# Kernel tuning notes

Measured on AMD Instinct MI355X. Metric: run time of the kernel, lower is better.

The kernel has to match this reference:

```python
import jax, jax.numpy as jnp
import numpy as np

N, E, C, A, R, HID = 10000, 160000, 128, 10, 8, 32
D_NODE = C * 4           # 128x0e + 128x1o -> 128 + 128*3
D_MID = 2 * C + 2 * C * 3  # irreps_mid = 2x128x0e + 2x128x1o -> 1024
AVG_NEIGH = 16.0
SQRT3 = 1.7320508075688772


def _linear_irreps(s, v, W0, W1):
    # e3nn-style per-irrep Linear: scalars [n,u]->[n,v], vectors [n,u,3]->[n,v,3]
    f = 1.0 / np.sqrt(W0.shape[0]).astype(np.float32)
    return s @ W0 * f, jnp.einsum('num,uv->nvm', v, W1) * f


def setup_inputs() -> dict:
    key = jax.random.key(0)
    ks = jax.random.split(key, 18)
    g = lambda i, sh: jax.random.normal(ks[i], sh, jnp.float32)
    return dict(
        node_attrs=g(0, (N, A)),
        node_feats=g(1, (N, D_NODE)),
        edge_attrs=g(2, (E, 4)),  # SH lmax=1: [Y00, Y1(-1..1)] (e3nn y,z,x order)
        edge_feats=jax.random.uniform(ks[3], (E, R), jnp.float32),
        edge_index=jax.random.randint(ks[4], (2, E), 0, N),
        W_up0=g(5, (C, C)), W_up1=g(6, (C, C)),
        Wr1=g(7, (R, 64)), Wr2=g(8, (64, 64)), Wr3=g(9, (64, 64)), Wr4=g(10, (64, 4 * C)),
        W_se1=g(11, (D_MID, HID)), W_se2=g(12, (HID, D_MID)),
        W_lin0=g(13, (2 * C, C)), W_lin1=g(14, (2 * C, C)),
        W_sk0=g(15, (C, A, C)), W_sk1=g(16, (C, A, C)),
    )


def reference(node_attrs, node_feats, edge_attrs, edge_feats, edge_index,
              W_up0, W_up1, Wr1, Wr2, Wr3, Wr4, W_se1, W_se2,
              W_lin0, W_lin1, W_sk0, W_sk1):
    n = node_feats.shape[0]
    e = edge_attrs.shape[0]
    s_in = node_feats[:, :C]
    v_in = node_feats[:, C:].reshape(n, C, 3)
    # linear_up (node_feats_irreps -> edge_irreps)
    s, v = _linear_irreps(s_in, v_in, W_up0, W_up1)
    # radial MLP (FullyConnectedNet, silu) -> per-edge TP weights [E, 4, C]
    h = edge_feats
    for W in (Wr1, Wr2, Wr3):
        h = jax.nn.silu(h @ W / np.sqrt(W.shape[0]).astype(np.float32))
    tpw = (h @ Wr4 / np.sqrt(Wr4.shape[0]).astype(np.float32)).reshape(e, 4, C)
    src, dst = edge_index[0], edge_index[1]
    ss, vv = s[src], v[src]          # gather source-node features per edge
    y0 = edge_attrs[:, 0]
    y1 = edge_attrs[:, 1:4]
    # equivariant TensorProduct (uvu, per-edge learned weights), 4 instructions
    m1 = tpw[:, 0] * ss * y0[:, None]                          # 0e x 0e -> 0e
    m2 = (tpw[:, 1] * ss)[:, :, None] * y1[:, None, :]         # 0e x 1o -> 1o
    m3 = tpw[:, 2][:, :, None] * vv * y0[:, None, None]        # 1o x 0e -> 1o
    m4 = tpw[:, 3] * jnp.einsum('eum,em->eu', vv, y1) / SQRT3  # 1o x 1o -> 0e
    S_m = jnp.concatenate([m1, m4], 1)       # [E, 2C] scalar part of irreps_mid
    V_m = jnp.concatenate([m2, m3], 1)       # [E, 2C, 3] vector part
    # SE attention gate on flattened edge messages (squeeze-excitation)
    mji = jnp.concatenate([S_m, V_m.reshape(e, -1)], 1)  # [E, 1024]
    gate = jax.nn.sigmoid(jax.nn.silu(mji @ W_se1) @ W_se2)
    mji = mji * gate
    S_m = mji[:, :2 * C]
    V_m = mji[:, 2 * C:].reshape(e, 2 * C, 3)
    # scatter-sum messages to destination nodes
    S_n = jax.ops.segment_sum(S_m, dst, num_segments=n)
    V_n = jax.ops.segment_sum(V_m, dst, num_segments=n)
    # linear (irreps_mid -> target), divided by avg_num_neighbors
    S_n, V_n = _linear_irreps(S_n, V_n, W_lin0, W_lin1)
    S_n = S_n / AVG_NEIGH
    V_n = V_n / AVG_NEIGH
    # skip_tp: FullyConnectedTensorProduct(target x 10x0e -> target)
    f = 1.0 / np.sqrt(C * A).astype(np.float32)
    S_o = jnp.einsum('nu,nw,uwv->nv', S_n, node_attrs, W_sk0) * f
    V_o = jnp.einsum('num,nw,uwv->nvm', V_n, node_attrs, W_sk1) * f
    # reshape_irreps -> [n, channels=C, 1+3]
    return jnp.concatenate([S_o[:, :, None], V_o], axis=2)
```

## Files before the change

### kernel.cpp

```cpp
#include <hip/hip_runtime.h>
#include <hip/hip_bf16.h>

#define N_NODES 10000
#define N_EDGES 160000

typedef __bf16 bf16x8 __attribute__((ext_vector_type(8)));
typedef float  f32x4  __attribute__((ext_vector_type(4)));
typedef unsigned short u16x8 __attribute__((ext_vector_type(8)));
union U16x8 { u16x8 u; bf16x8 b; };

__device__ __forceinline__ float sigf(float x){ return 1.0f/(1.0f+__expf(-x)); }
__device__ __forceinline__ float siluf(float x){ return x*sigf(x); }

__device__ __forceinline__ unsigned int f2bfbits(float f){
  unsigned int u = __float_as_uint(f);
  return (u + 0x7fffu + ((u>>16)&1u)) >> 16;
}
__device__ __forceinline__ void split3(float v, unsigned short* h, unsigned short* m, unsigned short* lo){
  unsigned int hb = f2bfbits(v); float hf = __uint_as_float(hb<<16);
  float r1 = v - hf;
  unsigned int mb = f2bfbits(r1); float mf = __uint_as_float(mb<<16);
  unsigned int lb = f2bfbits(r1 - mf);
  *h=(unsigned short)hb; *m=(unsigned short)mb; *lo=(unsigned short)lb;
}

__device__ __forceinline__ int dmap(int dp){
  int c = dp>>3, slot = dp&7;
  if (slot==0) return c;
  if (slot==1) return 128+c;
  if (slot<5)  return 256+3*c+(slot-2);
  return 640+3*c+(slot-5);
}

__global__ void pack_weights(const float* __restrict__ Wr4,
                             const float* __restrict__ Wse1,
                             const float* __restrict__ Wse2,
                             unsigned short* __restrict__ wr4pk,
                             unsigned short* __restrict__ wse1pk,
                             unsigned short* __restrict__ wse2pk)
{
  int t = blockIdx.x*256 + threadIdx.x;
  int j = t&7, l = (t>>3)&63;
  int lg = l>>4, lm = l&15;
  {
    int ks = (t>>9)&1; int nt = t>>10;
    int k = ks*32 + lg*8 + j;
    int col = nt*16 + lm;
    split3(Wr4[k*512+col]*0.125f, wr4pk+t, wr4pk+t+32768, wr4pk+t+65536);
  }
  {
    int kb = (t>>9)&31; int nt = t>>14;
    int d = dmap(kb*32 + lg*8 + j);
    int col = nt*16 + lm;
    split3(Wse1[d*32+col], wse1pk+t, wse1pk+t+32768, wse1pk+t+65536);
  }
  {
    int nt = t>>9;
    int krow = lg*8 + j;
    int d = dmap(nt*16 + lm);
    split3(Wse2[krow*1024+d], wse2pk+t, wse2pk+t+32768, wse2pk+t+65536);
  }
}

__global__ __launch_bounds__(128) void node_up_kernel(
    const float* __restrict__ nf, const float* __restrict__ W0, const float* __restrict__ W1,
    float* __restrict__ s_up, float* __restrict__ v_up)
{
  int n = blockIdx.x; int c = threadIdx.x;
  __shared__ float row[512];
  #pragma unroll
  for (int i=0;i<4;i++) row[c + 128*i] = nf[n*512 + c + 128*i];
  __syncthreads();
  float as=0.f, a0=0.f, a1=0.f, a2=0.f;
  for (int u=0;u<128;u++){
    float w0 = W0[u*128+c], w1 = W1[u*128+c];
    as += row[u]*w0;
    a0 += row[128+u*3+0]*w1;
    a1 += row[128+u*3+1]*w1;
    a2 += row[128+u*3+2]*w1;
  }
  const float f = 0.08838834764831845f;
  s_up[n*128+c] = as*f;
  v_up[n*384 + c*3+0] = a0*f;
  v_up[n*384 + c*3+1] = a1*f;
  v_up[n*384 + c*3+2] = a2*f;
}

#define OFF_MJI  16384
#define OFF_H3H  81920
#define OFF_H3L  83968
#define OFF_SG1H 86016
#define OFF_SG1L 87040
#define OFF_SRC  88064
#define OFF_DST  88128
#define OFF_Y    88192

__global__ __launch_bounds__(1024, 1) void edge_kernel(
    const float* __restrict__ ef, const float* __restrict__ ea, const int* __restrict__ ei,
    const float* __restrict__ Wr1, const float* __restrict__ Wr2, const float* __restrict__ Wr3,
    const unsigned short* __restrict__ wr4pk, const unsigned short* __restrict__ wse1pk,
    const unsigned short* __restrict__ wse2pk,
    const float* __restrict__ s_up, const float* __restrict__ v_up, float* __restrict__ accg)
{
  __shared__ __align__(16) char smem[88448];
  float* hA = (float*)smem;
  float* hB = (float*)(smem + 4096);
  float* partial = (float*)smem;
  int*   s_src = (int*)(smem + OFF_SRC);
  int*   s_dst = (int*)(smem + OFF_DST);
  float* s_y   = (float*)(smem + OFF_Y);

  const int t = threadIdx.x;
  const int e0 = blockIdx.x * 16;
  const int l = t & 63, w = t >> 6;
  const int lg = l >> 4, lm = l & 15;

  auto mjivec = [&](int v) -> float* {
    int p = v ^ ((v>>3)&7) ^ ((v>>8)&7);
    return (float*)(smem + OFF_MJI + p*16);
  };

  if (t < 16){ s_src[t] = ei[e0+t]; s_dst[t] = ei[N_EDGES + e0 + t]; }
  else if (t >= 64 && t < 128){ int q=t-64; s_y[(q>>2)*4 + (q&3)] = ea[(e0+(q>>2))*4 + (q&3)]; }

  {
    const int i = t & 63, eh = t >> 6;
    float r;
    { float a0=0.f;
      #pragma unroll
      for (int k=0;k<8;k++) a0 += ef[(e0+eh)*8+k]*Wr1[k*64+i];
      r = siluf(a0*0.35355339059327373f);
    }
    hA[eh*64+i]=r;
    __syncthreads();
    { float a0=0.f;
      for (int k=0;k<64;k++) a0 += hA[eh*64+k]*Wr2[k*64+i];
      r = siluf(a0*0.125f);
    }
    hB[eh*64+i]=r;
    __syncthreads();
    { float a0=0.f;
      for (int k=0;k<64;k++) a0 += hB[eh*64+k]*Wr3[k*64+i];
      r = siluf(a0*0.125f);
    }
    unsigned int hb = f2bfbits(r);
    unsigned int lb = f2bfbits(r - __uint_as_float(hb<<16));
    int o = (eh*128 + i*2) ^ ((eh&7)<<4);
    *(unsigned short*)(smem + OFF_H3H + o) = (unsigned short)hb;
    *(unsigned short*)(smem + OFF_H3L + o) = (unsigned short)lb;
  }
  __syncthreads();

  if (w < 8) {
    int oa0 = (lm*128 +  0 + lg*16) ^ ((lm&7)<<4);
    int oa1 = (lm*128 + 64 + lg*16) ^ ((lm&7)<<4);
    bf16x8 a0h = *(const bf16x8*)(smem + OFF_H3H + oa0);
    bf16x8 a1h = *(const bf16x8*)(smem + OFF_H3H + oa1);
    bf16x8 a0l = *(const bf16x8*)(smem + OFF_H3L + oa0);
    bf16x8 a1l = *(const bf16x8*)(smem + OFF_H3L + oa1);
    f32x4 tq[4];
    #pragma unroll
    for (int q=0;q<4;q++){
      int nt = q*8 + w;
      const unsigned short* bp0 = wr4pk + (nt*2+0)*512 + l*8;
      const unsigned short* bp1 = wr4pk + (nt*2+1)*512 + l*8;
      bf16x8 b0h = *(const bf16x8*)(bp0);
      bf16x8 b0m = *(const bf16x8*)(bp0+32768);
      bf16x8 b0l = *(const bf16x8*)(bp0+65536);
      bf16x8 b1h = *(const bf16x8*)(bp1);
      bf16x8 b1m = *(const bf16x8*)(bp1+32768);
      bf16x8 b1l = *(const bf16x8*)(bp1+65536);
      f32x4 acc = {0.f,0.f,0.f,0.f};
      acc = __builtin_amdgcn_mfma_f32_16x16x32_bf16(a0h,b0h,acc,0,0,0);
      acc = __builtin_amdgcn_mfma_f32_16x16x32_bf16(a1h,b1h,acc,0,0,0);
      acc = __builtin_amdgcn_mfma_f32_16x16x32_bf16(a0h,b0m,acc,0,0,0);
      acc = __builtin_amdgcn_mfma_f32_16x16x32_bf16(a1h,b1m,acc,0,0,0);
      acc = __builtin_amdgcn_mfma_f32_16x16x32_bf16(a0h,b0l,acc,0,0,0);
      acc = __builtin_amdgcn_mfma_f32_16x16x32_bf16(a1h,b1l,acc,0,0,0);
      acc = __builtin_amdgcn_mfma_f32_16x16x32_bf16(a0l,b0h,acc,0,0,0);
      acc = __builtin_amdgcn_mfma_f32_16x16x32_bf16(a1l,b1h,acc,0,0,0);
      acc = __builtin_amdgcn_mfma_f32_16x16x32_bf16(a0l,b0m,acc,0,0,0);
      acc = __builtin_amdgcn_mfma_f32_16x16x32_bf16(a1l,b1m,acc,0,0,0);
      tq[q] = acc;
    }
    const int cc = w*16 + lm;
    #pragma unroll
    for (int r=0;r<4;r++){
      int e = lg*4 + r;
      int src = s_src[e];
      float y0=s_y[e*4+0], yx=s_y[e*4+1], yy=s_y[e*4+2], yz=s_y[e*4+3];
      float ss = s_up[src*128+cc];
      const float* vp = v_up + src*384 + cc*3;
      float vx=vp[0], vy=vp[1], vz=vp[2];
      float m1  = tq[0][r]*ss*y0;
      float t1s = tq[1][r]*ss;
      float t2y = tq[2][r]*y0;
      float m4  = tq[3][r]*(vx*yx+vy*yy+vz*yz)*0.5773502691896258f;
      int v0 = e*256 + cc*2;
      f32x4 o0; o0[0]=m1;     o0[1]=m4;     o0[2]=t1s*yx; o0[3]=t1s*yy;
      f32x4 o1; o1[0]=t1s*yz; o1[1]=t2y*vx; o1[2]=t2y*vy; o1[3]=t2y*vz;
      *(f32x4*)mjivec(v0)   = o0;
      *(f32x4*)mjivec(v0+1) = o1;
    }
  }
  __syncthreads();

  if (w < 8) {
    f32x4 acc0 = {0.f,0.f,0.f,0.f}, acc1 = {0.f,0.f,0.f,0.f};
    #pragma unroll
    for (int ik=0; ik<4; ik++){
      int kb = w*4 + ik;
      int v = lm*256 + kb*8 + lg*2;
      f32x4 fa = *(const f32x4*)mjivec(v);
      f32x4 fb = *(const f32x4*)mjivec(v+1);
      U16x8 ua;
      ua.u[0]=(unsigned short)f2bfbits(fa[0]); ua.u[1]=(unsigned short)f2bfbits(fa[1]);
      ua.u[2]=(unsigned short)f2bfbits(fa[2]); ua.u[3]=(unsigned short)f2bfbits(fa[3]);
      ua.u[4]=(unsigned short)f2bfbits(fb[0]); ua.u[5]=(unsigned short)f2bfbits(fb[1]);
      ua.u[6]=(unsigned short)f2bfbits(fb[2]); ua.u[7]=(unsigned short)f2bfbits(fb[3]);
      bf16x8 a = ua.b;
      #pragma unroll
      for (int p=0;p<3;p++){
        bf16x8 b0 = *(const bf16x8*)(wse1pk + p*32768 + (0*32+kb)*512 + l*8);
        bf16x8 b1 = *(const bf16x8*)(wse1pk + p*32768 + (1*32+kb)*512 + l*8);
        acc0 = __builtin_amdgcn_mfma_f32_16x16x32_bf16(a,b0,acc0,0,0,0);
        acc1 = __builtin_amdgcn_mfma_f32_16x16x32_bf16(a,b1,acc1,0,0,0);
      }
    }
    #pragma unroll
    for (int r=0;r<4;r++){
      int row = lg*4 + r;
      partial[(w*16+row)*32 + lm     ] = acc0[r];
      partial[(w*16+row)*32 + 16+lm  ] = acc1[r];
    }
  }
  __syncthreads();
  if (t < 512) {
    int e = t>>5, jj = t&31;
    float s = 0.f;
    #pragma unroll
    for (int w8=0; w8<8; w8++) s += partial[(w8*16+e)*32 + jj];
    float g1 = siluf(s);
    unsigned int hb = f2bfbits(g1);
    unsigned int lb = f2bfbits(g1 - __uint_as_float(hb<<16));
    *(unsigned short*)(smem + OFF_SG1H + e*64 + jj*2) = (unsigned short)hb;
    *(unsigned short*)(smem + OFF_SG1L + e*64 + jj*2) = (unsigned short)lb;
  }
  __syncthreads();

  {
    bf16x8 ah = *(const bf16x8*)(smem + OFF_SG1H + lm*64 + lg*16);
    bf16x8 al = *(const bf16x8*)(smem + OFF_SG1L + lm*64 + lg*16);
    int de[4];
    #pragma unroll
    for (int r=0;r<4;r++) de[r] = s_dst[lg*4+r];
    #pragma unroll
    for (int nt4=0; nt4<4; nt4++){
      int nt = w*4 + nt4;
      const unsigned short* bp = wse2pk + nt*512 + l*8;
      bf16x8 b1 = *(const bf16x8*)(bp);
      bf16x8 b2 = *(const bf16x8*)(bp+32768);
      bf16x8 b3 = *(const bf16x8*)(bp+65536);
      f32x4 acc = {0.f,0.f,0.f,0.f};
      acc = __builtin_amdgcn_mfma_f32_16x16x32_bf16(ah,b1,acc,0,0,0);
      acc = __builtin_amdgcn_mfma_f32_16x16x32_bf16(ah,b2,acc,0,0,0);
      acc = __builtin_amdgcn_mfma_f32_16x16x32_bf16(ah,b3,acc,0,0,0);
      acc = __builtin_amdgcn_mfma_f32_16x16x32_bf16(al,b1,acc,0,0,0);
      acc = __builtin_amdgcn_mfma_f32_16x16x32_bf16(al,b2,acc,0,0,0);
      int col = nt*16 + lm;
      #pragma unroll
      for (int r=0;r<4;r++){
        int e = lg*4 + r;
        float gate = sigf(acc[r]);
        int word = e*1024 + col;
        float val = mjivec(word>>2)[word&3] * gate;
        unsafeAtomicAdd(accg + (size_t)de[r]*1024 + col, val);
      }
    }
  }
}

__global__ __launch_bounds__(512) void node_out_kernel(
    const float* __restrict__ acc, const float* __restrict__ na,
    const float* __restrict__ Wl0, const float* __restrict__ Wl1,
    const float* __restrict__ Wsk0, const float* __restrict__ Wsk1,
    float* __restrict__ out)
{
  __shared__ float sacc[8*1024];
  __shared__ float smid_s[8][128];
  __shared__ float smid_v[8][128][3];
  __shared__ float sattr[8][10];
  const int t = threadIdx.x;
  const int n0 = blockIdx.x*8;
  {
    const float4* src4 = (const float4*)(acc + (size_t)n0*1024);
    float4* dst4 = (float4*)sacc;
    for (int i=t;i<2048;i+=512) dst4[i] = src4[i];
  }
  if (t < 80) sattr[t/10][t%10] = na[n0*10 + t];
  __syncthreads();
  const int v2 = t & 127, ns = t >> 7;
  const float* acA = sacc + ns*1024;
  const float* acB = sacc + (ns+4)*1024;
  float sA=0.f, a0A=0.f, a1A=0.f, a2A=0.f;
  float sB=0.f, a0B=0.f, a1B=0.f, a2B=0.f;
  for (int u=0;u<128;u++){
    float w0  = Wl0[u*128+v2];
    float w1  = Wl1[u*128+v2];
    float w0b = Wl0[(128+u)*128+v2];
    float w1b = Wl1[(128+u)*128+v2];
    const float* a8 = acA + u*8;
    sA += a8[0]*w0;  sA += a8[1]*w0b;
    a0A += a8[2]*w1;  a1A += a8[3]*w1;  a2A += a8[4]*w1;
    a0A += a8[5]*w1b; a1A += a8[6]*w1b; a2A += a8[7]*w1b;
    const float* b8 = acB + u*8;
    sB += b8[0]*w0;  sB += b8[1]*w0b;
    a0B += b8[2]*w1;  a1B += b8[3]*w1;  a2B += b8[4]*w1;
    a0B += b8[5]*w1b; a1B += b8[6]*w1b; a2B += b8[7]*w1b;
  }
  const float fl = 0.00390625f;
  smid_s[ns][v2] = sA*fl;
  smid_v[ns][v2][0]=a0A*fl; smid_v[ns][v2][1]=a1A*fl; smid_v[ns][v2][2]=a2A*fl;
  smid_s[ns+4][v2] = sB*fl;
  smid_v[ns+4][v2][0]=a0B*fl; smid_v[ns+4][v2][1]=a1B*fl; smid_v[ns+4][v2][2]=a2B*fl;
  __syncthreads();
  float soA=0.f,o0A=0.f,o1A=0.f,o2A=0.f;
  float soB=0.f,o0B=0.f,o1B=0.f,o2B=0.f;
  for (int u=0;u<128;u++){
    float svA = smid_s[ns][u];
    float vA0 = smid_v[ns][u][0], vA1 = smid_v[ns][u][1], vA2 = smid_v[ns][u][2];
    float svB = smid_s[ns+4][u];
    float vB0 = smid_v[ns+4][u][0], vB1 = smid_v[ns+4][u][1], vB2 = smid_v[ns+4][u][2];
    const float* w0p = Wsk0 + u*1280 + v2;
    const float* w1p = Wsk1 + u*1280 + v2;
    #pragma unroll
    for (int wq=0;wq<10;wq++){
      float W0v = w0p[wq*128];
      float W1v = w1p[wq*128];
      float awA = sattr[ns][wq];
      float awB = sattr[ns+4][wq];
      soA += W0v*(svA*awA);
      o0A += W1v*(vA0*awA); o1A += W1v*(vA1*awA); o2A += W1v*(vA2*awA);
      soB += W0v*(svB*awB);
      o0B += W1v*(vB0*awB); o1B += W1v*(vB1*awB); o2B += W1v*(vB2*awB);
    }
  }
  const float fsk = 0.02795084971874737f;
  float4 oA; oA.x = soA*fsk; oA.y = o0A*fsk; oA.z = o1A*fsk; oA.w = o2A*fsk;
  *(float4*)(out + (size_t)(n0+ns)*512 + v2*4) = oA;
  float4 oB; oB.x = soB*fsk; oB.y = o0B*fsk; oB.z = o1B*fsk; oB.w = o2B*fsk;
  *(float4*)(out + (size_t)(n0+ns+4)*512 + v2*4) = oB;
}

extern "C" void kernel_launch(void* const* d_in, const int* in_sizes, int n_in,
                              void* d_out, int out_size, void* d_ws, size_t ws_size,
                              hipStream_t stream) {
  const float* node_attrs = (const float*)d_in[0];
  const float* node_feats = (const float*)d_in[1];
  const float* edge_attrs = (const float*)d_in[2];
  const float* edge_feats = (const float*)d_in[3];
  const int*   edge_index = (const int*)d_in[4];
  const float* W_up0 = (const float*)d_in[5];
  const float* W_up1 = (const float*)d_in[6];
  const float* Wr1   = (const float*)d_in[7];
  const float* Wr2   = (const float*)d_in[8];
  const float* Wr3   = (const float*)d_in[9];
  const float* Wr4   = (const float*)d_in[10];
  const float* W_se1 = (const float*)d_in[11];
  const float* W_se2 = (const float*)d_in[12];
  const float* W_lin0= (const float*)d_in[13];
  const float* W_lin1= (const float*)d_in[14];
  const float* W_sk0 = (const float*)d_in[15];
  const float* W_sk1 = (const float*)d_in[16];

  float* ws   = (float*)d_ws;
  float* accg = ws;
  float* s_up = ws + 10240000;
  float* v_up = s_up + 1280000;
  unsigned short* wr4pk  = (unsigned short*)(v_up + 3840000);
  unsigned short* wse1pk = wr4pk + 98304;
  unsigned short* wse2pk = wse1pk + 98304;

  hipMemsetAsync(accg, 0, (size_t)10240000*4, stream);
  pack_weights<<<128, 256, 0, stream>>>(Wr4, W_se1, W_se2, wr4pk, wse1pk, wse2pk);
  node_up_kernel<<<N_NODES, 128, 0, stream>>>(node_feats, W_up0, W_up1, s_up, v_up);
  edge_kernel<<<N_EDGES/16, 1024, 0, stream>>>(edge_feats, edge_attrs, edge_index,
      Wr1, Wr2, Wr3, wr4pk, wse1pk, wse2pk, s_up, v_up, accg);
  node_out_kernel<<<N_NODES/8, 512, 0, stream>>>(accg, node_attrs,
      W_lin0, W_lin1, W_sk0, W_sk1, (float*)d_out);
}
```

Baseline: 1.119 ms.

## Use readlane radial MLP and LDS atomics to cut barriers and use all waves

Each wave now handles one edge of the radial MLP and broadcasts hidden activations with readlane instead of staging them through shared memory. This removes two block barriers and the hA/hB buffers. The SE first-layer GEMM is split across all 16 waves instead of 8, and the cross-wave partial sums are reduced with shared-memory atomicAdd into a zeroed 16x32 buffer. Shared memory shrinks and launch bounds change, but LDS float atomics add contention and make the accumulation order nondeterministic.

```diff
diff --git a/kernel.cpp b/kernel.cpp
--- a/kernel.cpp
+++ b/kernel.cpp
@@ -22,6 +22,9 @@
   unsigned int mb = f2bfbits(r1); float mf = __uint_as_float(mb<<16);
   unsigned int lb = f2bfbits(r1 - mf);
   *h=(unsigned short)hb; *m=(unsigned short)mb; *lo=(unsigned short)lb;
+}
+__device__ __forceinline__ float rdlane(float v, int k){
+  return __uint_as_float(__builtin_amdgcn_readlane(__float_as_uint(v), k));
 }
 
 __device__ __forceinline__ int dmap(int dp){
@@ -86,26 +89,25 @@
   v_up[n*384 + c*3+2] = a2*f;
 }
 
-#define OFF_MJI  16384
-#define OFF_H3H  81920
-#define OFF_H3L  83968
-#define OFF_SG1H 86016
-#define OFF_SG1L 87040
-#define OFF_SRC  88064
-#define OFF_DST  88128
-#define OFF_Y    88192
-
-__global__ __launch_bounds__(1024, 1) void edge_kernel(
+#define OFF_MJI  0
+#define OFF_H3H  65536
+#define OFF_H3L  67584
+#define OFF_PART 69632
+#define OFF_SG1H 71680
+#define OFF_SG1L 72704
+#define OFF_SRC  73728
+#define OFF_DST  73792
+#define OFF_Y    73856
+
+__global__ __launch_bounds__(1024, 8) void edge_kernel(
     const float* __restrict__ ef, const float* __restrict__ ea, const int* __restrict__ ei,
     const float* __restrict__ Wr1, const float* __restrict__ Wr2, const float* __restrict__ Wr3,
     const unsigned short* __restrict__ wr4pk, const unsigned short* __restrict__ wse1pk,
     const unsigned short* __restrict__ wse2pk,
     const float* __restrict__ s_up, const float* __restrict__ v_up, float* __restrict__ accg)
 {
-  __shared__ __align__(16) char smem[88448];
-  float* hA = (float*)smem;
-  float* hB = (float*)(smem + 4096);
-  float* partial = (float*)smem;
+  __shared__ __align__(16) char smem[74112];
+  float* partial = (float*)(smem + OFF_PART);
   int*   s_src = (int*)(smem + OFF_SRC);
   int*   s_dst = (int*)(smem + OFF_DST);
   float* s_y   = (float*)(smem + OFF_Y);
@@ -122,30 +124,35 @@
 
   if (t < 16){ s_src[t] = ei[e0+t]; s_dst[t] = ei[N_EDGES + e0 + t]; }
   else if (t >= 64 && t < 128){ int q=t-64; s_y[(q>>2)*4 + (q&3)] = ea[(e0+(q>>2))*4 + (q&3)]; }
-
-  {
-    const int i = t & 63, eh = t >> 6;
-    float r;
-    { float a0=0.f;
-      #pragma unroll
-      for (int k=0;k<8;k++) a0 += ef[(e0+eh)*8+k]*Wr1[k*64+i];
-      r = siluf(a0*0.35355339059327373f);
-    }
-    hA[eh*64+i]=r;
-    __syncthreads();
-    { float a0=0.f;
-      for (int k=0;k<64;k++) a0 += hA[eh*64+k]*Wr2[k*64+i];
-      r = siluf(a0*0.125f);
-    }
-    hB[eh*64+i]=r;
-    __syncthreads();
-    { float a0=0.f;
-      for (int k=0;k<64;k++) a0 += hB[eh*64+k]*Wr3[k*64+i];
-      r = siluf(a0*0.125f);
-    }
-    unsigned int hb = f2bfbits(r);
-    unsigned int lb = f2bfbits(r - __uint_as_float(hb<<16));
-    int o = (eh*128 + i*2) ^ ((eh&7)<<4);
+  if (t < 512) partial[t] = 0.f;
+
+  {
+    const int i = l;
+    float a0=0.f;
+    #pragma unroll
+    for (int k=0;k<8;k++) a0 += ef[(e0+w)*8+k]*Wr1[k*64+i];
+    float r = siluf(a0*0.35355339059327373f);
+    float b0=0.f,b1=0.f,b2=0.f,b3=0.f;
+    #pragma unroll
+    for (int k=0;k<64;k+=4){
+      b0 += rdlane(r, k+0)*Wr2[(k+0)*64+i];
+      b1 += rdlane(r, k+1)*Wr2[(k+1)*64+i];
+      b2 += rdlane(r, k+2)*Wr2[(k+2)*64+i];
+      b3 += rdlane(r, k+3)*Wr2[(k+3)*64+i];
+    }
+    float r2 = siluf(((b0+b1)+(b2+b3))*0.125f);
+    b0=b1=b2=b3=0.f;
+    #pragma unroll
+    for (int k=0;k<64;k+=4){
+      b0 += rdlane(r2, k+0)*Wr3[(k+0)*64+i];
+      b1 += rdlane(r2, k+1)*Wr3[(k+1)*64+i];
+      b2 += rdlane(r2, k+2)*Wr3[(k+2)*64+i];
+      b3 += rdlane(r2, k+3)*Wr3[(k+3)*64+i];
+    }
+    float r3 = siluf(((b0+b1)+(b2+b3))*0.125f);
+    unsigned int hb = f2bfbits(r3);
+    unsigned int lb = f2bfbits(r3 - __uint_as_float(hb<<16));
+    int o = (w*128 + i*2) ^ ((w&7)<<4);
     *(unsigned short*)(smem + OFF_H3H + o) = (unsigned short)hb;
     *(unsigned short*)(smem + OFF_H3L + o) = (unsigned short)lb;
   }
@@ -205,11 +212,11 @@
   }
   __syncthreads();
 
-  if (w < 8) {
+  {
     f32x4 acc0 = {0.f,0.f,0.f,0.f}, acc1 = {0.f,0.f,0.f,0.f};
     #pragma unroll
-    for (int ik=0; ik<4; ik++){
-      int kb = w*4 + ik;
+    for (int ik=0; ik<2; ik++){
+      int kb = w*2 + ik;
       int v = lm*256 + kb*8 + lg*2;
       f32x4 fa = *(const f32x4*)mjivec(v);
       f32x4 fb = *(const f32x4*)mjivec(v+1);
@@ -230,17 +237,14 @@
     #pragma unroll
     for (int r=0;r<4;r++){
       int row = lg*4 + r;
-      partial[(w*16+row)*32 + lm     ] = acc0[r];
-      partial[(w*16+row)*32 + 16+lm  ] = acc1[r];
+      atomicAdd(partial + row*32 + lm,      acc0[r]);
+      atomicAdd(partial + row*32 + 16 + lm, acc1[r]);
     }
   }
   __syncthreads();
   if (t < 512) {
     int e = t>>5, jj = t&31;
-    float s = 0.f;
-    #pragma unroll
-    for (int w8=0; w8<8; w8++) s += partial[(w8*16+e)*32 + jj];
-    float g1 = siluf(s);
+    float g1 = siluf(partial[e*32+jj]);
     unsigned int hb = f2bfbits(g1);
     unsigned int lb = f2bfbits(g1 - __uint_as_float(hb<<16));
     *(unsigned short*)(smem + OFF_SG1H + e*64 + jj*2) = (unsigned short)hb;
```

Result: slower. 1.294 ms (+15.7%).

## Sort edges by destination and pre-reduce messages in-block before atomics

Applied to the files above, without the earlier changes.

Adds a counting sort of edges by destination node (histogram, scan, scatter into a permutation). The edge kernel then processes edges in sorted order and writes the gated messages back to shared memory. Runs of edges with the same destination within a 16-edge block are summed per column before a single atomic add. This is meant to cut global atomic traffic. The cost is three extra small kernels and indirect, uncoalesced gathers of edge features and attributes.

```diff
diff --git a/kernel.cpp b/kernel.cpp
--- a/kernel.cpp
+++ b/kernel.cpp
@@ -30,6 +30,45 @@
   if (slot==1) return 128+c;
   if (slot<5)  return 256+3*c+(slot-2);
   return 640+3*c+(slot-5);
+}
+
+__global__ void hist_kernel(const int* __restrict__ ei, int* __restrict__ hist){
+  int e = blockIdx.x*256 + threadIdx.x;
+  if (e < N_EDGES) atomicAdd(&hist[ei[N_EDGES+e]], 1);
+}
+
+__global__ __launch_bounds__(1024) void scan_kernel(const int* __restrict__ hist, int* __restrict__ cursor){
+  __shared__ int lsum[2][1024];
+  const int t = threadIdx.x;
+  int s = 0;
+  if (t < 1000){
+    #pragma unroll
+    for (int i=0;i<10;i++) s += hist[t*10+i];
+  }
+  lsum[0][t] = s;
+  __syncthreads();
+  int src = 0;
+  for (int off=1; off<1024; off<<=1){
+    int v = lsum[src][t];
+    if (t >= off) v += lsum[src][t-off];
+    lsum[src^1][t] = v;
+    __syncthreads();
+    src ^= 1;
+  }
+  if (t < 1000){
+    int run = t ? lsum[src][t-1] : 0;
+    #pragma unroll
+    for (int i=0;i<10;i++){ cursor[t*10+i] = run; run += hist[t*10+i]; }
+  }
+}
+
+__global__ void scatter_kernel(const int* __restrict__ ei, int* __restrict__ cursor, int* __restrict__ perm){
+  int e = blockIdx.x*256 + threadIdx.x;
+  if (e < N_EDGES){
+    int d = ei[N_EDGES+e];
+    int pos = atomicAdd(&cursor[d], 1);
+    perm[pos] = e;
+  }
 }
 
 __global__ void pack_weights(const float* __restrict__ Wr4,
@@ -97,6 +136,7 @@
 
 __global__ __launch_bounds__(1024, 1) void edge_kernel(
     const float* __restrict__ ef, const float* __restrict__ ea, const int* __restrict__ ei,
+    const int* __restrict__ perm,
     const float* __restrict__ Wr1, const float* __restrict__ Wr2, const float* __restrict__ Wr3,
     const unsigned short* __restrict__ wr4pk, const unsigned short* __restrict__ wse1pk,
     const unsigned short* __restrict__ wse2pk,
@@ -120,15 +160,20 @@
     return (float*)(smem + OFF_MJI + p*16);
   };
 
-  if (t < 16){ s_src[t] = ei[e0+t]; s_dst[t] = ei[N_EDGES + e0 + t]; }
-  else if (t >= 64 && t < 128){ int q=t-64; s_y[(q>>2)*4 + (q&3)] = ea[(e0+(q>>2))*4 + (q&3)]; }
+  if (t < 16){ int pe = perm[e0+t]; s_src[t] = ei[pe]; s_dst[t] = ei[N_EDGES + pe]; }
+  else if (t >= 64 && t < 128){
+    int q = t-64;
+    int pe = perm[e0 + (q>>2)];
+    s_y[(q>>2)*4 + (q&3)] = ea[pe*4 + (q&3)];
+  }
 
   {
     const int i = t & 63, eh = t >> 6;
+    int pe = perm[e0 + eh];
     float r;
     { float a0=0.f;
       #pragma unroll
-      for (int k=0;k<8;k++) a0 += ef[(e0+eh)*8+k]*Wr1[k*64+i];
+      for (int k=0;k<8;k++) a0 += ef[pe*8+k]*Wr1[k*64+i];
       r = siluf(a0*0.35355339059327373f);
     }
     hA[eh*64+i]=r;
@@ -251,9 +296,6 @@
   {
     bf16x8 ah = *(const bf16x8*)(smem + OFF_SG1H + lm*64 + lg*16);
     bf16x8 al = *(const bf16x8*)(smem + OFF_SG1L + lm*64 + lg*16);
-    int de[4];
-    #pragma unroll
-    for (int r=0;r<4;r++) de[r] = s_dst[lg*4+r];
     #pragma unroll
     for (int nt4=0; nt4<4; nt4++){
       int nt = w*4 + nt4;
@@ -273,10 +315,30 @@
         int e = lg*4 + r;
         float gate = sigf(acc[r]);
         int word = e*1024 + col;
-        float val = mjivec(word>>2)[word&3] * gate;
-        unsafeAtomicAdd(accg + (size_t)de[r]*1024 + col, val);
+        float* p = mjivec(word>>2) + (word&3);
+        *p = *p * gate;
       }
     }
+  }
+  __syncthreads();
+
+  {
+    const int dp = t;
+    int cur = s_dst[0];
+    int w0 = dp;
+    float run = mjivec(w0>>2)[w0&3];
+    #pragma unroll
+    for (int e=1;e<16;e++){
+      int d = s_dst[e];
+      int wd = e*1024 + dp;
+      float v = mjivec(wd>>2)[wd&3];
+      if (d == cur) run += v;
+      else {
+        unsafeAtomicAdd(accg + (size_t)cur*1024 + dp, run);
+        cur = d; run = v;
+      }
+    }
+    unsafeAtomicAdd(accg + (size_t)cur*1024 + dp, run);
   }
 }
 
@@ -380,11 +442,18 @@
   unsigned short* wr4pk  = (unsigned short*)(v_up + 3840000);
   unsigned short* wse1pk = wr4pk + 98304;
   unsigned short* wse2pk = wse1pk + 98304;
+  int* hist   = (int*)(wse2pk + 98304);
+  int* cursor = hist + 10000;
+  int* perm   = cursor + 10000;
 
   hipMemsetAsync(accg, 0, (size_t)10240000*4, stream);
+  hipMemsetAsync(hist, 0, 10000*4, stream);
+  hist_kernel<<<(N_EDGES+255)/256, 256, 0, stream>>>(edge_index, hist);
+  scan_kernel<<<1, 1024, 0, stream>>>(hist, cursor);
+  scatter_kernel<<<(N_EDGES+255)/256, 256, 0, stream>>>(edge_index, cursor, perm);
   pack_weights<<<128, 256, 0, stream>>>(Wr4, W_se1, W_se2, wr4pk, wse1pk, wse2pk);
   node_up_kernel<<<N_NODES, 128, 0, stream>>>(node_feats, W_up0, W_up1, s_up, v_up);
-  edge_kernel<<<N_EDGES/16, 1024, 0, stream>>>(edge_feats, edge_attrs, edge_index,
+  edge_kernel<<<N_EDGES/16, 1024, 0, stream>>>(edge_feats, edge_attrs, edge_index, perm,
       Wr1, Wr2, Wr3, wr4pk, wse1pk, wse2pk, s_up, v_up, accg);
   node_out_kernel<<<N_NODES/8, 512, 0, stream>>>(accg, node_attrs,
       W_lin0, W_lin1, W_sk0, W_sk1, (float*)d_out);
```

Result: faster. 1.083 ms, median of 3 (-3.2%).
